# Kernel optimization log

Hardware: AMD Instinct MI355X
Metric: run time of the kernel (lower is better)

Reference implementation:

```python
import jax, jax.numpy as jnp
import numpy as np

N = 20000      # nodes
E = 320000     # edges (before self loops)
HID = 128      # args.hidden
HEADS = 8
C1 = HID // 2  # 64, gat1 out per head -> 512 concat
C2 = HID // 4  # 32, gat2 out per head -> 256 concat
D1 = HEADS * C1  # 512
D2 = HEADS * C2  # 256
JKD = HID + D1 + D2  # 896


def _glorot(key, shape):
    fan_in, fan_out = shape[0], shape[-1]
    s = jnp.sqrt(6.0 / (fan_in + fan_out))
    return jax.random.uniform(key, shape, jnp.float32, -s, s)


def setup_inputs() -> dict:
    key = jax.random.key(0)
    ks = jax.random.split(key, 18)
    x = jax.random.normal(ks[0], (N, HID), jnp.float32)
    edge_index = jax.random.randint(ks[1], (2, E), 0, N, dtype=jnp.int32)
    return {
        "x": x,
        "edge_index": edge_index,
        # GATv2 layer 1
        "Wl1": _glorot(ks[2], (HID, D1)), "bl1": jnp.zeros((D1,), jnp.float32),
        "Wr1": _glorot(ks[3], (HID, D1)), "br1": jnp.zeros((D1,), jnp.float32),
        "att1": _glorot(ks[4], (HEADS, C1)),
        "bias1": jnp.zeros((D1,), jnp.float32),
        # GATv2 layer 2
        "Wl2": _glorot(ks[5], (D1, D2)), "bl2": jnp.zeros((D2,), jnp.float32),
        "Wr2": _glorot(ks[6], (D1, D2)), "br2": jnp.zeros((D2,), jnp.float32),
        "att2": _glorot(ks[7], (HEADS, C2)),
        "bias2": jnp.zeros((D2,), jnp.float32),
        # JK linear
        "Wjk": _glorot(ks[8], (JKD, HID)), "bjk": jnp.zeros((HID,), jnp.float32),
    }


def gatv2_layer(x, src, dst, Wl, bl, Wr, br, att, bias, n):
    """PyG GATv2Conv (concat=True, eval mode: no dropout), neg_slope=0.2."""
    H, C = att.shape
    xl = (x @ Wl + bl).reshape(n, H, C)  # source transform (messages)
    xr = (x @ Wr + br).reshape(n, H, C)  # target transform
    e = jax.nn.leaky_relu(xl[src] + xr[dst], 0.2)        # [E,H,C]
    logits = jnp.einsum('ehc,hc->eh', e, att)            # [E,H]
    # numerically stable segment softmax over incoming edges per dst node
    m = jax.ops.segment_max(logits, dst, num_segments=n) # [N,H]
    a = jnp.exp(logits - m[dst])
    denom = jax.ops.segment_sum(a, dst, num_segments=n)
    alpha = a / denom[dst]                               # [E,H]
    out = jax.ops.segment_sum(alpha[:, :, None] * xl[src], dst, num_segments=n)
    return out.reshape(n, H * C) + bias


def reference(x, edge_index, Wl1, bl1, Wr1, br1, att1, bias1,
              Wl2, bl2, Wr2, br2, att2, bias2, Wjk, bjk):
    n = x.shape[0]
    loop = jnp.arange(n, dtype=edge_index.dtype)
    src = jnp.concatenate([edge_index[0], loop])  # add self loops (PyG default)
    dst = jnp.concatenate([edge_index[1], loop])

    jk0 = x
    h1 = jax.nn.elu(gatv2_layer(x, src, dst, Wl1, bl1, Wr1, br1, att1, bias1, n))
    h2 = jax.nn.elu(gatv2_layer(h1, src, dst, Wl2, bl2, Wr2, br2, att2, bias2, n))
    jk = jnp.concatenate([jk0, h1, h2], axis=-1)  # JumpingKnowledge('cat')
    return jk @ Wjk + bjk
```

## Files before the change

### kernel.cpp

```cpp
#include <hip/hip_runtime.h>

typedef unsigned short u16;
typedef __attribute__((ext_vector_type(8))) short bf16x8;
typedef __attribute__((ext_vector_type(4))) float f32x4;

__device__ __forceinline__ float bf2f(u16 u) { return __uint_as_float(((unsigned)u) << 16); }
__device__ __forceinline__ u16 f2bf(float f) {
  unsigned u = __float_as_uint(f);
  u += 0x7fffu + ((u >> 16) & 1u);
  return (u16)(u >> 16);
}
__device__ __forceinline__ void bf2x2(unsigned w, float& lo, float& hi) {
  lo = __uint_as_float(w << 16);
  hi = __uint_as_float(w & 0xffff0000u);
}
__device__ __forceinline__ unsigned pk2(float lo, float hi) {
  return (unsigned)f2bf(lo) | ((unsigned)f2bf(hi) << 16);
}

__device__ __forceinline__ float red8(float p) {
  p += __int_as_float(__builtin_amdgcn_ds_swizzle(__float_as_int(p), 0x041F));
  p += __int_as_float(__builtin_amdgcn_ds_swizzle(__float_as_int(p), 0x081F));
  p += __int_as_float(__builtin_amdgcn_ds_swizzle(__float_as_int(p), 0x101F));
  return p;
}
__device__ __forceinline__ float red4(float p) {
  p += __int_as_float(__builtin_amdgcn_ds_swizzle(__float_as_int(p), 0x041F));
  p += __int_as_float(__builtin_amdgcn_ds_swizzle(__float_as_int(p), 0x081F));
  return p;
}

__global__ __launch_bounds__(256) void prepw_kernel(
    const float* __restrict__ x,
    const float* __restrict__ bl1, const float* __restrict__ br1,
    const float* __restrict__ bl2, const float* __restrict__ br2,
    const float* __restrict__ Wl1, const float* __restrict__ Wr1,
    const float* __restrict__ Wl2, const float* __restrict__ Wr2,
    const float* __restrict__ Wjk,
    u16* __restrict__ XH, float* __restrict__ BC1, float* __restrict__ BC2,
    int* __restrict__ cur, u16* __restrict__ Wp,
    int nx, int total, int prepBlocks)
{
  if (blockIdx.x < prepBlocks) {
    int i = blockIdx.x * 256 + threadIdx.x;
    if (i >= total) return;
    if (i < nx) { XH[i] = f2bf(x[i]); return; }
    int j = i - nx;
    if (j < 1024) { BC1[j] = (j < 512) ? bl1[j] : br1[j - 512]; return; }
    if (j < 1536) { int t = j - 1024; BC2[t] = (t < 256) ? bl2[t] : br2[t - 256]; return; }
    cur[j - 1536] = 0;
    return;
  }
  __shared__ float T[64][65];
  int t = blockIdx.x - prepBlocks;
  const float *Wa, *Wb; int Nhalf, lds, k0, n0, KsT, SUBS; size_t obase; bool split;
  if (t < 32) {
    int kt = t & 1, nt = t >> 1;
    k0 = kt * 64; n0 = nt * 64; obase = 0; KsT = 4; SUBS = 8; split = true;
    Wa = Wl1; Wb = Wr1; Nhalf = 512; lds = 512;
  } else if (t < 96) {
    int tt = t - 32; int kt = tt & 7, nt = tt >> 3;
    k0 = kt * 64; n0 = nt * 64; obase = 262144; KsT = 16; SUBS = 8; split = true;
    Wa = Wl2; Wb = Wr2; Nhalf = 256; lds = 256;
  } else {
    int tt = t - 96; int kt = tt % 14, nt = tt / 14;
    k0 = kt * 64; n0 = nt * 64; obase = 786432; KsT = 28; SUBS = 4; split = false;
    Wa = Wjk; Wb = nullptr; Nhalf = 128; lds = 128;
  }
  const int tid = threadIdx.x;
  const int lane = tid & 63, unit = tid >> 6;
  {
    int n = n0 + lane;
    const float* S = (n < Nhalf) ? Wa : Wb;
    int nn = (n < Nhalf) ? n : n - Nhalf;
#pragma unroll
    for (int r = 0; r < 16; ++r) {
      int kl = unit + 4 * r;
      T[kl][lane] = S[(size_t)(k0 + kl) * lds + nn];
    }
  }
  __syncthreads();
  const int tn = n0 >> 6;
#pragma unroll
  for (int u = 0; u < 2; ++u) {
    int c = unit * 2 + u;
    int ks_l = c >> 2, nc = c & 3;
    int ksg = (k0 >> 5) + ks_l;
    size_t ob = obase + ((size_t)(tn * KsT + ksg) * SUBS + nc) * 512 + lane * 8;
#pragma unroll
    for (int j = 0; j < 8; ++j) {
      float v = T[ks_l * 32 + (lane >> 4) * 8 + j][nc * 16 + (lane & 15)];
      u16 h = f2bf(v);
      Wp[ob + j] = h;
      if (split) Wp[ob + 2048 + j] = f2bf(v - bf2f(h));
    }
  }
}

__global__ __launch_bounds__(256) void hist_kernel(
    const int* __restrict__ ei, int E, int ET, int* __restrict__ cnt)
{
  int e = blockIdx.x * 256 + threadIdx.x;
  if (e >= ET) return;
  int d = (e < E) ? ei[E + e] : (e - E);
  atomicAdd(&cnt[d], 1);
}

__global__ __launch_bounds__(1024) void scan_kernel(
    int* __restrict__ cnt, int* __restrict__ rowptr, int n)
{
  __shared__ int wsum[16];
  __shared__ int carry;
  const int tid = threadIdx.x, lane = tid & 63, wv = tid >> 6;
  if (tid == 0) carry = 0;
  __syncthreads();
  for (int base = 0; base < n; base += 1024) {
    int i = base + tid;
    int v = (i < n) ? cnt[i] : 0;
    if (i < n) cnt[i] = 0;
    int s = v;
#pragma unroll
    for (int ofs = 1; ofs < 64; ofs <<= 1) {
      int t = __shfl_up(s, ofs);
      if (lane >= ofs) s += t;
    }
    if (lane == 63) wsum[wv] = s;
    __syncthreads();
    if (wv == 0 && lane < 16) {
      int t = wsum[lane];
#pragma unroll
      for (int ofs = 1; ofs < 16; ofs <<= 1) {
        int u = __shfl_up(t, ofs);
        if (lane >= ofs) t += u;
      }
      wsum[lane] = t;
    }
    __syncthreads();
    int waveoff = (wv == 0) ? 0 : wsum[wv - 1];
    if (i < n) rowptr[i] = carry + waveoff + s - v;
    int tot = wsum[15];
    __syncthreads();
    if (tid == 0) carry += tot;
    __syncthreads();
  }
  if (threadIdx.x == 0) rowptr[n] = carry;
}

template<int MROWS, int NW, bool SPLIT, bool BF16OUT>
__device__ __forceinline__ void gemmct_body(
    u16* __restrict__ ldsA, int bid,
    const u16* __restrict__ A0, int lda0, int K0,
    const u16* __restrict__ A1, int lda1, int K1,
    const u16* __restrict__ A2, int lda2, int K2,
    const u16* __restrict__ Wp, int KsT,
    int kof0, int kof1, int kof2,
    const float* __restrict__ bias,
    void* __restrict__ Cv, int ldc, int M, int N)
{
  constexpr int SUBS = SPLIT ? 8 : 4;
  const int tid  = threadIdx.x;
  const int lane = tid & 63;
  const int wv   = tid >> 6;
  const int quad = lane >> 4;
  const int r16  = lane & 15;
  const int m0   = bid * MROWS;

  const u16* As[3]   = {A0, A1, A2};
  const int  Ks[3]   = {K0, K1, K2};
  const int  ldas[3] = {lda0, lda1, lda2};
  const int  kofs[3] = {kof0, kof1, kof2};

  int soff[3];
  int so = 0;
#pragma unroll
  for (int s = 0; s < 3; ++s) {
    const int K = Ks[s];
    soff[s] = so;
    if (K == 0) continue;
    const int stride = K + 8;
    const int cpr = K >> 3;
    const int sh  = 32 - __clz(cpr - 1);
    const int tot = MROWS << sh;
    for (int c = tid; c < tot; c += NW * 64) {
      int row = c >> sh, kc = c & ((1 << sh) - 1);
      if (kc < cpr) {
        int sr = m0 + row; if (sr >= M) sr = M - 1;
        uint4 v = *reinterpret_cast<const uint4*>(As[s] + (size_t)sr * ldas[s] + kc * 8);
        *reinterpret_cast<uint4*>(&ldsA[so + row * stride + kc * 8]) = v;
      }
    }
    so += MROWS * stride;
  }
  __syncthreads();

  constexpr int MM = MROWS / 16;
  for (int n0w = wv * 64; n0w < N; n0w += NW * 64) {
    const int t = n0w >> 6;
    f32x4 acc[MM][4];
#pragma unroll
    for (int mm = 0; mm < MM; ++mm)
#pragma unroll
      for (int nc = 0; nc < 4; ++nc) acc[mm][nc] = (f32x4){0.f, 0.f, 0.f, 0.f};

#pragma unroll
    for (int s = 0; s < 3; ++s) {
      const int K = Ks[s];
      if (K == 0) continue;
      const int stride = K + 8;
      const int ksb = kofs[s] >> 5;
      const u16* lbase = &ldsA[soff[s] + r16 * stride + quad * 8];

#pragma unroll 2
      for (int k0 = 0; k0 < K; k0 += 32) {
        const int ks = ksb + (k0 >> 5);
        const u16* ch = Wp + (((size_t)(t * KsT + ks) * SUBS) << 9) + lane * 8;
        bf16x8 af[MM];
#pragma unroll
        for (int mm = 0; mm < MM; ++mm)
          af[mm] = *reinterpret_cast<const bf16x8*>(lbase + mm * 16 * stride + k0);
        bf16x8 whf[4], wlf[4];
#pragma unroll
        for (int nc = 0; nc < 4; ++nc) {
          whf[nc] = *reinterpret_cast<const bf16x8*>(ch + (nc << 9));
          if (SPLIT) wlf[nc] = *reinterpret_cast<const bf16x8*>(ch + ((4 + nc) << 9));
        }
#pragma unroll
        for (int mm = 0; mm < MM; ++mm)
#pragma unroll
          for (int nc = 0; nc < 4; ++nc) {
            acc[mm][nc] = __builtin_amdgcn_mfma_f32_16x16x32_bf16(whf[nc], af[mm], acc[mm][nc], 0, 0, 0);
            if (SPLIT)
              acc[mm][nc] = __builtin_amdgcn_mfma_f32_16x16x32_bf16(wlf[nc], af[mm], acc[mm][nc], 0, 0, 0);
          }
      }
    }

#pragma unroll
    for (int mm = 0; mm < MM; ++mm) {
      const int m = m0 + mm * 16 + r16;
      if (m >= M) continue;
#pragma unroll
      for (int nc = 0; nc < 4; ++nc) {
        const int n = n0w + nc * 16 + quad * 4;
        float b0 = 0.f, b1 = 0.f, b2 = 0.f, b3 = 0.f;
        if (bias) {
          float4 bv = *reinterpret_cast<const float4*>(bias + n);
          b0 = bv.x; b1 = bv.y; b2 = bv.z; b3 = bv.w;
        }
        float v0 = acc[mm][nc][0] + b0;
        float v1 = acc[mm][nc][1] + b1;
        float v2 = acc[mm][nc][2] + b2;
        float v3 = acc[mm][nc][3] + b3;
        if (BF16OUT) {
          ushort4 o = { f2bf(v0), f2bf(v1), f2bf(v2), f2bf(v3) };
          *reinterpret_cast<ushort4*>((u16*)Cv + (size_t)m * ldc + n) = o;
        } else {
          float4 o = { v0, v1, v2, v3 };
          *reinterpret_cast<float4*>((float*)Cv + (size_t)m * ldc + n) = o;
        }
      }
    }
  }
}

template<int MROWS, int NW, int WPE, bool SPLIT, bool BF16OUT, int LDSU16>
__global__ __launch_bounds__(NW * 64, WPE) void gemmct_kernel(
    const u16* __restrict__ A0, int lda0, int K0,
    const u16* __restrict__ A1, int lda1, int K1,
    const u16* __restrict__ A2, int lda2, int K2,
    const u16* __restrict__ Wp, int KsT,
    int kof0, int kof1, int kof2,
    const float* __restrict__ bias,
    void* __restrict__ Cv, int ldc, int M, int N)
{
  __shared__ u16 ldsA[LDSU16];
  gemmct_body<MROWS, NW, SPLIT, BF16OUT>(
      ldsA, blockIdx.x, A0, lda0, K0, A1, lda1, K1, A2, lda2, K2,
      Wp, KsT, kof0, kof1, kof2, bias, Cv, ldc, M, N);
}

template<int MROWS, int NW, int WPE, bool SPLIT, bool BF16OUT, int LDSU16>
__global__ __launch_bounds__(NW * 64, WPE) void gemm1_scatter_kernel(
    const u16* __restrict__ A0, int lda0, int K0,
    const u16* __restrict__ Wp, int KsT,
    const float* __restrict__ bias,
    void* __restrict__ Cv, int ldc, int M, int N, int gemmBlocks,
    const int* __restrict__ ei, int E, int ET,
    const int* __restrict__ rowptr, int* __restrict__ cur, int* __restrict__ srcs)
{
  __shared__ u16 ldsA[LDSU16];
  if ((int)blockIdx.x < gemmBlocks) {
    gemmct_body<MROWS, NW, SPLIT, BF16OUT>(
        ldsA, blockIdx.x, A0, lda0, K0, nullptr, 0, 0, nullptr, 0, 0,
        Wp, KsT, 0, 0, 0, bias, Cv, ldc, M, N);
    return;
  }
  int e = ((int)blockIdx.x - gemmBlocks) * (NW * 64) + (int)threadIdx.x;
  if (e >= ET) return;
  int s, d;
  if (e < E) { s = ei[e]; d = ei[E + e]; } else { s = e - E; d = s; }
  int pos = rowptr[d] + atomicAdd(&cur[d], 1);
  srcs[pos] = s;
}

template<int VPL>
__device__ __forceinline__ void load_row(const u16* p, float* dst) {
  if constexpr (VPL == 8) {
    uint4 t = *reinterpret_cast<const uint4*>(p);
    bf2x2(t.x, dst[0], dst[1]); bf2x2(t.y, dst[2], dst[3]);
    bf2x2(t.z, dst[4], dst[5]); bf2x2(t.w, dst[6], dst[7]);
  } else {
    uint2 t = *reinterpret_cast<const uint2*>(p);
    bf2x2(t.x, dst[0], dst[1]); bf2x2(t.y, dst[2], dst[3]);
  }
}

__global__ __launch_bounds__(256) void gath1_kernel(
    const u16* __restrict__ XLR,
    const int* __restrict__ rowptr, const int* __restrict__ srcs,
    const float* __restrict__ att, const float* __restrict__ bias,
    u16* __restrict__ Hh, int Nn)
{
  const int tid   = threadIdx.x;
  const int s     = tid & 7;
  const int gib   = tid >> 3;
  const int head  = blockIdx.x & 7;
  const int chunk = blockIdx.x >> 3;
  const int nch   = gridDim.x >> 3;

  const int hoff = head * 64 + s * 8;

  float c1[8], c2[8], biasR[8];
#pragma unroll
  for (int w = 0; w < 8; ++w) {
    float a = att[hoff + w];
    c1[w] = 0.6f * a;
    c2[w] = 0.4f * a;
    biasR[w] = bias[hoff + w];
  }

  for (int d = chunk * 32 + gib; d < Nn; d += nch * 32) {
    float xr[8];
    load_row<8>(XLR + (size_t)d * 1024 + 512 + hoff, xr);
    const int jb = rowptr[d], je = rowptr[d + 1];

    float acc[8];
    load_row<8>(XLR + (size_t)srcs[jb] * 1024 + hoff, acc);
    float p0 = 0.f;
#pragma unroll
    for (int w = 0; w < 8; ++w) {
      float v = acc[w] + xr[w];
      p0 = fmaf(c1[w], v, fmaf(c2[w], fabsf(v), p0));
    }
    p0 = red8(p0);
    float den = 1.f;

    int j = jb + 1;
    for (; j + 1 < je; j += 2) {
      float xa[8], xb[8];
      load_row<8>(XLR + (size_t)srcs[j]     * 1024 + hoff, xa);
      load_row<8>(XLR + (size_t)srcs[j + 1] * 1024 + hoff, xb);
      float pa = 0.f, pb = 0.f;
#pragma unroll
      for (int w = 0; w < 8; ++w) {
        float va = xa[w] + xr[w];
        float vb = xb[w] + xr[w];
        pa = fmaf(c1[w], va, fmaf(c2[w], fabsf(va), pa));
        pb = fmaf(c1[w], vb, fmaf(c2[w], fabsf(vb), pb));
      }
      pa = red8(pa); pb = red8(pb);
      const float ea = __expf(pa - p0);
      const float eb = __expf(pb - p0);
      den += ea + eb;
#pragma unroll
      for (int w = 0; w < 8; ++w)
        acc[w] = fmaf(ea, xa[w], fmaf(eb, xb[w], acc[w]));
    }
    if (j < je) {
      float xa[8];
      load_row<8>(XLR + (size_t)srcs[j] * 1024 + hoff, xa);
      float pa = 0.f;
#pragma unroll
      for (int w = 0; w < 8; ++w) {
        float va = xa[w] + xr[w];
        pa = fmaf(c1[w], va, fmaf(c2[w], fabsf(va), pa));
      }
      pa = red8(pa);
      const float ea = __expf(pa - p0);
      den += ea;
#pragma unroll
      for (int w = 0; w < 8; ++w) acc[w] = fmaf(ea, xa[w], acc[w]);
    }

    const float inv = 1.f / den;
    float o[8];
#pragma unroll
    for (int w = 0; w < 8; ++w) {
      float v = fmaf(acc[w], inv, biasR[w]);
      o[w] = v > 0.f ? v : (__expf(v) - 1.f);
    }
    uint4 ov = { pk2(o[0], o[1]), pk2(o[2], o[3]), pk2(o[4], o[5]), pk2(o[6], o[7]) };
    *reinterpret_cast<uint4*>(Hh + (size_t)d * 512 + hoff) = ov;
  }
}

__global__ __launch_bounds__(256) void gath2_kernel(
    const u16* __restrict__ XLR,
    const int* __restrict__ rowptr, const int* __restrict__ srcs,
    const float* __restrict__ att, const float* __restrict__ bias,
    u16* __restrict__ Hh, int Nn)
{
  const int tid   = threadIdx.x;
  const int s     = tid & 3;
  const int gib   = tid >> 2;
  const int head  = blockIdx.x & 7;
  const int chunk = blockIdx.x >> 3;
  const int nch   = gridDim.x >> 3;

  const int hoff = head * 32 + s * 8;

  float c1[8], c2[8], biasR[8];
#pragma unroll
  for (int w = 0; w < 8; ++w) {
    float a = att[hoff + w];
    c1[w] = 0.6f * a;
    c2[w] = 0.4f * a;
    biasR[w] = bias[hoff + w];
  }

  for (int d = chunk * 64 + gib; d < Nn; d += nch * 64) {
    float xr[8];
    load_row<8>(XLR + (size_t)d * 512 + 256 + hoff, xr);
    const int jb = rowptr[d], je = rowptr[d + 1];

    float acc[8];
    load_row<8>(XLR + (size_t)srcs[jb] * 512 + hoff, acc);
    float p0 = 0.f;
#pragma unroll
    for (int w = 0; w < 8; ++w) {
      float v = acc[w] + xr[w];
      p0 = fmaf(c1[w], v, fmaf(c2[w], fabsf(v), p0));
    }
    p0 = red4(p0);
    float den = 1.f;

    int j = jb + 1;
    for (; j + 1 < je; j += 2) {
      float xa[8], xb[8];
      load_row<8>(XLR + (size_t)srcs[j]     * 512 + hoff, xa);
      load_row<8>(XLR + (size_t)srcs[j + 1] * 512 + hoff, xb);
      float pa = 0.f, pb = 0.f;
#pragma unroll
      for (int w = 0; w < 8; ++w) {
        float va = xa[w] + xr[w];
        float vb = xb[w] + xr[w];
        pa = fmaf(c1[w], va, fmaf(c2[w], fabsf(va), pa));
        pb = fmaf(c1[w], vb, fmaf(c2[w], fabsf(vb), pb));
      }
      pa = red4(pa); pb = red4(pb);
      const float ea = __expf(pa - p0);
      const float eb = __expf(pb - p0);
      den += ea + eb;
#pragma unroll
      for (int w = 0; w < 8; ++w)
        acc[w] = fmaf(ea, xa[w], fmaf(eb, xb[w], acc[w]));
    }
    if (j < je) {
      float xa[8];
      load_row<8>(XLR + (size_t)srcs[j] * 512 + hoff, xa);
      float pa = 0.f;
#pragma unroll
      for (int w = 0; w < 8; ++w) {
        float va = xa[w] + xr[w];
        pa = fmaf(c1[w], va, fmaf(c2[w], fabsf(va), pa));
      }
      pa = red4(pa);
      const float ea = __expf(pa - p0);
      den += ea;
#pragma unroll
      for (int w = 0; w < 8; ++w) acc[w] = fmaf(ea, xa[w], acc[w]);
    }

    const float inv = 1.f / den;
    float o[8];
#pragma unroll
    for (int w = 0; w < 8; ++w) {
      float v = fmaf(acc[w], inv, biasR[w]);
      o[w] = v > 0.f ? v : (__expf(v) - 1.f);
    }
    uint4 ov = { pk2(o[0], o[1]), pk2(o[2], o[3]), pk2(o[4], o[5]), pk2(o[6], o[7]) };
    *reinterpret_cast<uint4*>(Hh + (size_t)d * 256 + hoff) = ov;
  }
}


extern "C" void kernel_launch(void* const* d_in, const int* in_sizes, int n_in,
                              void* d_out, int out_size, void* d_ws, size_t ws_size,
                              hipStream_t stream) {
  const float* x     = (const float*)d_in[0];
  const int*   ei    = (const int*)d_in[1];
  const float* Wl1   = (const float*)d_in[2];
  const float* bl1   = (const float*)d_in[3];
  const float* Wr1   = (const float*)d_in[4];
  const float* br1   = (const float*)d_in[5];
  const float* att1  = (const float*)d_in[6];
  const float* bias1 = (const float*)d_in[7];
  const float* Wl2   = (const float*)d_in[8];
  const float* bl2   = (const float*)d_in[9];
  const float* Wr2   = (const float*)d_in[10];
  const float* br2   = (const float*)d_in[11];
  const float* att2  = (const float*)d_in[12];
  const float* bias2 = (const float*)d_in[13];
  const float* Wjk   = (const float*)d_in[14];
  const float* bjk   = (const float*)d_in[15];
  float* out = (float*)d_out;

  const int Nn = in_sizes[0] / 128;
  const int E  = in_sizes[1] / 2;
  const int ET = E + Nn;

  const size_t nx = (size_t)Nn * 128;

  const size_t oW1  = 0;
  const size_t oW2  = 262144;
  const size_t oWjk = 786432;
  const size_t npack = 901120;

  char* ws = (char*)d_ws;
  size_t off = 0;
  u16* XH = (u16*)(ws + off); off += nx * 2;
  u16* Wp = (u16*)(ws + off); off += npack * 2;
  float* BC1 = (float*)(ws + off); off += 1024 * 4;
  float* BC2 = (float*)(ws + off); off += 512 * 4;
  u16* XLR1 = (u16*)(ws + off);
  u16* XLR2 = XLR1;
  off += (size_t)Nn * 1024 * 2;
  u16* H1h = (u16*)(ws + off); off += (size_t)Nn * 512 * 2;
  u16* H2h = (u16*)(ws + off); off += (size_t)Nn * 256 * 2;
  int* rowptr = (int*)(ws + off); off += (size_t)(Nn + 1) * 4;
  int* cur    = (int*)(ws + off); off += (size_t)Nn * 4;
  int* srcs   = (int*)(ws + off); off += (size_t)ET * 4;

  const int nprep = (int)(nx + 1536 + Nn);
  const int prepBlocks = (nprep + 255) / 256;
  prepw_kernel<<<prepBlocks + 124, 256, 0, stream>>>(
      x, bl1, br1, bl2, br2, Wl1, Wr1, Wl2, Wr2, Wjk,
      XH, BC1, BC2, cur, Wp, (int)nx, nprep, prepBlocks);
  hist_kernel<<<(ET + 255) / 256, 256, 0, stream>>>(ei, E, ET, cur);
  scan_kernel<<<1, 1024, 0, stream>>>(cur, rowptr, Nn);

  const int g1blocks = (Nn + 31) / 32;
  const int scatBlocks = (ET + 511) / 512;
  gemm1_scatter_kernel<32, 8, 4, true, true, 32 * 136>
      <<<g1blocks + scatBlocks, 512, 0, stream>>>(
      XH, 128, 128,
      Wp + oW1, 4, BC1,
      XLR1, 1024, Nn, 1024, g1blocks,
      ei, E, ET, rowptr, cur, srcs);
  gath1_kernel<<<5000, 256, 0, stream>>>(
      XLR1, rowptr, srcs, att1, bias1, H1h, Nn);

  gemmct_kernel<48, 8, 4, true, true, 48 * 520>
      <<<(Nn + 47) / 48, 512, 0, stream>>>(
      H1h, 512, 512, nullptr, 0, 0, nullptr, 0, 0,
      Wp + oW2, 16, 0, 0, 0, BC2,
      XLR2, 512, Nn, 512);
  gath2_kernel<<<2504, 256, 0, stream>>>(
      XLR2, rowptr, srcs, att2, bias2, H2h, Nn);

  gemmct_kernel<16, 2, 1, false, false, 16 * 920>
      <<<(Nn + 15) / 16, 128, 0, stream>>>(
      XH, 128, 128, H1h, 512, 512, H2h, 256, 256,
      Wp + oWjk, 28, 0, 128, 640, bjk,
      out, 128, Nn, 128);
}
```

Measured before the change: 298.9 us.

## Sort destination nodes by in-degree to balance gather kernel work

After: 300.3 us. About the same (+0.5%).

```diff
diff --git a/kernel.cpp b/kernel.cpp
--- a/kernel.cpp
+++ b/kernel.cpp
@@ -107,17 +107,24 @@
 }
 
 __global__ __launch_bounds__(1024) void scan_kernel(
-    int* __restrict__ cnt, int* __restrict__ rowptr, int n)
+    int* __restrict__ cnt, int* __restrict__ rowptr, int* __restrict__ perm,
+    int n)
 {
   __shared__ int wsum[16];
   __shared__ int carry;
+  __shared__ int dh[64];
+  __shared__ int dbase[64];
   const int tid = threadIdx.x, lane = tid & 63, wv = tid >> 6;
   if (tid == 0) carry = 0;
+  if (tid < 64) dh[tid] = 0;
   __syncthreads();
   for (int base = 0; base < n; base += 1024) {
     int i = base + tid;
     int v = (i < n) ? cnt[i] : 0;
-    if (i < n) cnt[i] = 0;
+    if (i < n) {
+      cnt[i] = 0;
+      atomicAdd(&dh[v < 63 ? v : 63], 1);
+    }
     int s = v;
 #pragma unroll
     for (int ofs = 1; ofs < 64; ofs <<= 1) {
@@ -143,7 +150,24 @@
     if (tid == 0) carry += tot;
     __syncthreads();
   }
-  if (threadIdx.x == 0) rowptr[n] = carry;
+  if (tid == 0) rowptr[n] = carry;
+  __syncthreads();
+  if (tid == 0) {
+    int s = 0;
+    for (int k = 63; k >= 0; --k) { dbase[k] = s; s += dh[k]; }
+  }
+  __syncthreads();
+  if (tid < 64) dh[tid] = 0;
+  __syncthreads();
+  for (int base = 0; base < n; base += 1024) {
+    int i = base + tid;
+    if (i < n) {
+      int deg = rowptr[i + 1] - rowptr[i];
+      int b = deg < 63 ? deg : 63;
+      int pos = dbase[b] + atomicAdd(&dh[b], 1);
+      perm[pos] = i;
+    }
+  }
 }
 
 template<int MROWS, int NW, bool SPLIT, bool BF16OUT>
@@ -318,6 +342,7 @@
 __global__ __launch_bounds__(256) void gath1_kernel(
     const u16* __restrict__ XLR,
     const int* __restrict__ rowptr, const int* __restrict__ srcs,
+    const int* __restrict__ perm,
     const float* __restrict__ att, const float* __restrict__ bias,
     u16* __restrict__ Hh, int Nn)
 {
@@ -326,7 +351,10 @@
   const int gib   = tid >> 3;
   const int head  = blockIdx.x & 7;
   const int chunk = blockIdx.x >> 3;
-  const int nch   = gridDim.x >> 3;
+
+  const int idx = chunk * 32 + gib;
+  if (idx >= Nn) return;
+  const int d = perm[idx];
 
   const int hoff = head * 64 + s * 8;
 
@@ -339,74 +367,73 @@
     biasR[w] = bias[hoff + w];
   }
 
-  for (int d = chunk * 32 + gib; d < Nn; d += nch * 32) {
-    float xr[8];
-    load_row<8>(XLR + (size_t)d * 1024 + 512 + hoff, xr);
-    const int jb = rowptr[d], je = rowptr[d + 1];
-
-    float acc[8];
-    load_row<8>(XLR + (size_t)srcs[jb] * 1024 + hoff, acc);
-    float p0 = 0.f;
+  float xr[8];
+  load_row<8>(XLR + (size_t)d * 1024 + 512 + hoff, xr);
+  const int jb = rowptr[d], je = rowptr[d + 1];
+
+  float acc[8];
+  load_row<8>(XLR + (size_t)srcs[jb] * 1024 + hoff, acc);
+  float p0 = 0.f;
+#pragma unroll
+  for (int w = 0; w < 8; ++w) {
+    float v = acc[w] + xr[w];
+    p0 = fmaf(c1[w], v, fmaf(c2[w], fabsf(v), p0));
+  }
+  p0 = red8(p0);
+  float den = 1.f;
+
+  int j = jb + 1;
+  for (; j + 1 < je; j += 2) {
+    float xa[8], xb[8];
+    load_row<8>(XLR + (size_t)srcs[j]     * 1024 + hoff, xa);
+    load_row<8>(XLR + (size_t)srcs[j + 1] * 1024 + hoff, xb);
+    float pa = 0.f, pb = 0.f;
 #pragma unroll
     for (int w = 0; w < 8; ++w) {
-      float v = acc[w] + xr[w];
-      p0 = fmaf(c1[w], v, fmaf(c2[w], fabsf(v), p0));
-    }
-    p0 = red8(p0);
-    float den = 1.f;
-
-    int j = jb + 1;
-    for (; j + 1 < je; j += 2) {
-      float xa[8], xb[8];
-      load_row<8>(XLR + (size_t)srcs[j]     * 1024 + hoff, xa);
-      load_row<8>(XLR + (size_t)srcs[j + 1] * 1024 + hoff, xb);
-      float pa = 0.f, pb = 0.f;
-#pragma unroll
-      for (int w = 0; w < 8; ++w) {
-        float va = xa[w] + xr[w];
-        float vb = xb[w] + xr[w];
-        pa = fmaf(c1[w], va, fmaf(c2[w], fabsf(va), pa));
-        pb = fmaf(c1[w], vb, fmaf(c2[w], fabsf(vb), pb));
-      }
-      pa = red8(pa); pb = red8(pb);
-      const float ea = __expf(pa - p0);
-      const float eb = __expf(pb - p0);
-      den += ea + eb;
-#pragma unroll
-      for (int w = 0; w < 8; ++w)
-        acc[w] = fmaf(ea, xa[w], fmaf(eb, xb[w], acc[w]));
-    }
-    if (j < je) {
-      float xa[8];
-      load_row<8>(XLR + (size_t)srcs[j] * 1024 + hoff, xa);
-      float pa = 0.f;
-#pragma unroll
-      for (int w = 0; w < 8; ++w) {
-        float va = xa[w] + xr[w];
-        pa = fmaf(c1[w], va, fmaf(c2[w], fabsf(va), pa));
-      }
-      pa = red8(pa);
-      const float ea = __expf(pa - p0);
-      den += ea;
-#pragma unroll
-      for (int w = 0; w < 8; ++w) acc[w] = fmaf(ea, xa[w], acc[w]);
-    }
-
-    const float inv = 1.f / den;
-    float o[8];
+      float va = xa[w] + xr[w];
+      float vb = xb[w] + xr[w];
+      pa = fmaf(c1[w], va, fmaf(c2[w], fabsf(va), pa));
+      pb = fmaf(c1[w], vb, fmaf(c2[w], fabsf(vb), pb));
+    }
+    pa = red8(pa); pb = red8(pb);
+    const float ea = __expf(pa - p0);
+    const float eb = __expf(pb - p0);
+    den += ea + eb;
+#pragma unroll
+    for (int w = 0; w < 8; ++w)
+      acc[w] = fmaf(ea, xa[w], fmaf(eb, xb[w], acc[w]));
+  }
+  if (j < je) {
+    float xa[8];
+    load_row<8>(XLR + (size_t)srcs[j] * 1024 + hoff, xa);
+    float pa = 0.f;
 #pragma unroll
     for (int w = 0; w < 8; ++w) {
-      float v = fmaf(acc[w], inv, biasR[w]);
-      o[w] = v > 0.f ? v : (__expf(v) - 1.f);
-    }
-    uint4 ov = { pk2(o[0], o[1]), pk2(o[2], o[3]), pk2(o[4], o[5]), pk2(o[6], o[7]) };
-    *reinterpret_cast<uint4*>(Hh + (size_t)d * 512 + hoff) = ov;
-  }
+      float va = xa[w] + xr[w];
+      pa = fmaf(c1[w], va, fmaf(c2[w], fabsf(va), pa));
+    }
+    pa = red8(pa);
+    const float ea = __expf(pa - p0);
+    den += ea;
+#pragma unroll
+    for (int w = 0; w < 8; ++w) acc[w] = fmaf(ea, xa[w], acc[w]);
+  }
+
+  const float inv = 1.f / den;
+  float o[8];
+#pragma unroll
+  for (int w = 0; w < 8; ++w) {
+    float v = fmaf(acc[w], inv, biasR[w]);
+    o[w] = v > 0.f ? v : (__expf(v) - 1.f);
+  }
+  uint4 ov = { pk2(o[0], o[1]), pk2(o[2], o[3]), pk2(o[4], o[5]), pk2(o[6], o[7]) };
+  *reinterpret_cast<uint4*>(Hh + (size_t)d * 512 + hoff) = ov;
 }
 
 __global__ __launch_bounds__(256) void gath2_kernel(
     const u16* __restrict__ XLR,
     const int* __restrict__ rowptr, const int* __restrict__ srcs,
+    const int* __restrict__ perm,
     const float* __restrict__ att, const float* __restrict__ bias,
     u16* __restrict__ Hh, int Nn)
 {
@@ -415,7 +442,10 @@
   const int gib   = tid >> 2;
   const int head  = blockIdx.x & 7;
   const int chunk = blockIdx.x >> 3;
-  const int nch   = gridDim.x >> 3;
+
+  const int idx = chunk * 64 + gib;
+  if (idx >= Nn) return;
+  const int d = perm[idx];
 
   const int hoff = head * 32 + s * 8;
 
@@ -428,69 +458,67 @@
     biasR[w] = bias[hoff + w];
   }
 
-  for (int d = chunk * 64 + gib; d < Nn; d += nch * 64) {
-    float xr[8];
-    load_row<8>(XLR + (size_t)d * 512 + 256 + hoff, xr);
-    const int jb = rowptr[d], je = rowptr[d + 1];
-
-    float acc[8];
-    load_row<8>(XLR + (size_t)srcs[jb] * 512 + hoff, acc);
-    float p0 = 0.f;
+  float xr[8];
+  load_row<8>(XLR + (size_t)d * 512 + 256 + hoff, xr);
+  const int jb = rowptr[d], je = rowptr[d + 1];
+
+  float acc[8];
+  load_row<8>(XLR + (size_t)srcs[jb] * 512 + hoff, acc);
+  float p0 = 0.f;
+#pragma unroll
+  for (int w = 0; w < 8; ++w) {
+    float v = acc[w] + xr[w];
+    p0 = fmaf(c1[w], v, fmaf(c2[w], fabsf(v), p0));
+  }
+  p0 = red4(p0);
+  float den = 1.f;
+
+  int j = jb + 1;
+  for (; j + 1 < je; j += 2) {
+    float xa[8], xb[8];
+    load_row<8>(XLR + (size_t)srcs[j]     * 512 + hoff, xa);
+    load_row<8>(XLR + (size_t)srcs[j + 1] * 512 + hoff, xb);
+    float pa = 0.f, pb = 0.f;
 #pragma unroll
     for (int w = 0; w < 8; ++w) {
-      float v = acc[w] + xr[w];
-      p0 = fmaf(c1[w], v, fmaf(c2[w], fabsf(v), p0));
-    }
-    p0 = red4(p0);
-    float den = 1.f;
-
-    int j = jb + 1;
-    for (; j + 1 < je; j += 2) {
-      float xa[8], xb[8];
-      load_row<8>(XLR + (size_t)srcs[j]     * 512 + hoff, xa);
-      load_row<8>(XLR + (size_t)srcs[j + 1] * 512 + hoff, xb);
-      float pa = 0.f, pb = 0.f;
-#pragma unroll
-      for (int w = 0; w < 8; ++w) {
-        float va = xa[w] + xr[w];
-        float vb = xb[w] + xr[w];
-        pa = fmaf(c1[w], va, fmaf(c2[w], fabsf(va), pa));
-        pb = fmaf(c1[w], vb, fmaf(c2[w], fabsf(vb), pb));
-      }
-      pa = red4(pa); pb = red4(pb);
-      const float ea = __expf(pa - p0);
-      const float eb = __expf(pb - p0);
-      den += ea + eb;
-#pragma unroll
-      for (int w = 0; w < 8; ++w)
-        acc[w] = fmaf(ea, xa[w], fmaf(eb, xb[w], acc[w]));
-    }
-    if (j < je) {
-      float xa[8];
-      load_row<8>(XLR + (size_t)srcs[j] * 512 + hoff, xa);
-      float pa = 0.f;
-#pragma unroll
-      for (int w = 0; w < 8; ++w) {
-        float va = xa[w] + xr[w];
-        pa = fmaf(c1[w], va, fmaf(c2[w], fabsf(va), pa));
-      }
-      pa = red4(pa);
-      const float ea = __expf(pa - p0);
-      den += ea;
-#pragma unroll
-      for (int w = 0; w < 8; ++w) acc[w] = fmaf(ea, xa[w], acc[w]);
-    }
-
-    const float inv = 1.f / den;
-    float o[8];
+      float va = xa[w] + xr[w];
+      float vb = xb[w] + xr[w];
+      pa = fmaf(c1[w], va, fmaf(c2[w], fabsf(va), pa));
+      pb = fmaf(c1[w], vb, fmaf(c2[w], fabsf(vb), pb));
+    }
+    pa = red4(pa); pb = red4(pb);
+    const float ea = __expf(pa - p0);
+    const float eb = __expf(pb - p0);
+    den += ea + eb;
+#pragma unroll
+    for (int w = 0; w < 8; ++w)
+      acc[w] = fmaf(ea, xa[w], fmaf(eb, xb[w], acc[w]));
+  }
+  if (j < je) {
+    float xa[8];
+    load_row<8>(XLR + (size_t)srcs[j] * 512 + hoff, xa);
+    float pa = 0.f;
 #pragma unroll
     for (int w = 0; w < 8; ++w) {
-      float v = fmaf(acc[w], inv, biasR[w]);
-      o[w] = v > 0.f ? v : (__expf(v) - 1.f);
-    }
-    uint4 ov = { pk2(o[0], o[1]), pk2(o[2], o[3]), pk2(o[4], o[5]), pk2(o[6], o[7]) };
-    *reinterpret_cast<uint4*>(Hh + (size_t)d * 256 + hoff) = ov;
-  }
+      float va = xa[w] + xr[w];
+      pa = fmaf(c1[w], va, fmaf(c2[w], fabsf(va), pa));
+    }
+    pa = red4(pa);
+    const float ea = __expf(pa - p0);
+    den += ea;
+#pragma unroll
+    for (int w = 0; w < 8; ++w) acc[w] = fmaf(ea, xa[w], acc[w]);
+  }
+
+  const float inv = 1.f / den;
+  float o[8];
+#pragma unroll
+  for (int w = 0; w < 8; ++w) {
+    float v = fmaf(acc[w], inv, biasR[w]);
+    o[w] = v > 0.f ? v : (__expf(v) - 1.f);
+  }
+  uint4 ov = { pk2(o[0], o[1]), pk2(o[2], o[3]), pk2(o[4], o[5]), pk2(o[6], o[7]) };
+  *reinterpret_cast<uint4*>(Hh + (size_t)d * 256 + hoff) = ov;
 }
 
 
@@ -539,6 +567,7 @@
   u16* H2h = (u16*)(ws + off); off += (size_t)Nn * 256 * 2;
   int* rowptr = (int*)(ws + off); off += (size_t)(Nn + 1) * 4;
   int* cur    = (int*)(ws + off); off += (size_t)Nn * 4;
+  int* perm   = (int*)(ws + off); off += (size_t)Nn * 4;
   int* srcs   = (int*)(ws + off); off += (size_t)ET * 4;
 
   const int nprep = (int)(nx + 1536 + Nn);
@@ -547,7 +576,7 @@
       x, bl1, br1, bl2, br2, Wl1, Wr1, Wl2, Wr2, Wjk,
       XH, BC1, BC2, cur, Wp, (int)nx, nprep, prepBlocks);
   hist_kernel<<<(ET + 255) / 256, 256, 0, stream>>>(ei, E, ET, cur);
-  scan_kernel<<<1, 1024, 0, stream>>>(cur, rowptr, Nn);
+  scan_kernel<<<1, 1024, 0, stream>>>(cur, rowptr, perm, Nn);
 
   const int g1blocks = (Nn + 31) / 32;
   const int scatBlocks = (ET + 511) / 512;
@@ -558,7 +587,7 @@
       XLR1, 1024, Nn, 1024, g1blocks,
       ei, E, ET, rowptr, cur, srcs);
   gath1_kernel<<<5000, 256, 0, stream>>>(
-      XLR1, rowptr, srcs, att1, bias1, H1h, Nn);
+      XLR1, rowptr, srcs, perm, att1, bias1, H1h, Nn);
 
   gemmct_kernel<48, 8, 4, true, true, 48 * 520>
       <<<(Nn + 47) / 48, 512, 0, stream>>>(
@@ -566,7 +595,7 @@
       Wp + oW2, 16, 0, 0, 0, BC2,
       XLR2, 512, Nn, 512);
   gath2_kernel<<<2504, 256, 0, stream>>>(
-      XLR2, rowptr, srcs, att2, bias2, H2h, Nn);
+      XLR2, rowptr, srcs, perm, att2, bias2, H2h, Nn);
 
   gemmct_kernel<16, 2, 1, false, false, 16 * 920>
       <<<(Nn + 15) / 16, 128, 0, stream>>>(
```
